# Performance work log

Hardware: AMD Instinct MI355X
Metric: run time of the kernel (lower is better)

The kernel has to match this reference:

```python
import jax, jax.numpy as jnp
import numpy as np

BATCH, N, DIM_IN, DIM_K, DIM_V, NH = 2, 4096, 256, 256, 256, 8

def setup_inputs() -> dict:
    key = jax.random.key(0)
    k1, k2, k3, k4 = jax.random.split(key, 4)
    s = 1.0 / np.sqrt(DIM_IN)
    return {
        "x": jax.random.normal(k1, (BATCH, N, DIM_IN), dtype=jnp.float32),
        "Wq": jax.random.normal(k2, (DIM_IN, DIM_K), dtype=jnp.float32) * s,
        "Wk": jax.random.normal(k3, (DIM_IN, DIM_K), dtype=jnp.float32) * s,
        "Wv": jax.random.normal(k4, (DIM_IN, DIM_V), dtype=jnp.float32) * s,
    }

def reference(x, Wq, Wk, Wv):
    b, n, _ = x.shape
    nh = NH
    dk = DIM_K // nh
    dv = DIM_V // nh
    # project and split heads: [b, nh, n, dk]
    q = jnp.einsum('bni,ik->bnk', x, Wq).reshape(b, n, nh, dk).transpose(0, 2, 1, 3)
    k = jnp.einsum('bni,ik->bnk', x, Wk).reshape(b, n, nh, dk).transpose(0, 2, 1, 3)
    v = jnp.einsum('bni,iv->bnv', x, Wv).reshape(b, n, nh, dv).transpose(0, 2, 1, 3)
    scale = 1.0 / np.sqrt(dk)
    dist = jnp.einsum('bhqd,bhkd->bhqk', q, k) * scale  # [b, nh, n, n]
    dist = jax.nn.softmax(dist, axis=-1)
    # dropout is identity in eval mode
    att = jnp.einsum('bhqk,bhkv->bhqv', dist, v)  # [b, nh, n, dv]
    return att.transpose(0, 2, 1, 3).reshape(b, n, DIM_V)
```

## Files before the change

### kernel.cpp

```cpp
#include <hip/hip_runtime.h>
#include <math.h>

#define BATCH 2
#define SEQ   4096
#define DIN   256
#define NH    8
#define DH    32
#define BH    (BATCH*NH)
#define NSPLIT 8
#define KRANGE (SEQ/NSPLIT)
#define TILES  (KRANGE/64)
#define QTILE  256

typedef short bf16x8 __attribute__((ext_vector_type(8)));
typedef float f32x4  __attribute__((ext_vector_type(4)));

#if defined(__has_builtin)
#if __has_builtin(__builtin_amdgcn_exp2f)
#define EXP2(x) __builtin_amdgcn_exp2f(x)
#else
#define EXP2_ASM 1
#endif
#else
#define EXP2_ASM 1
#endif
#ifdef EXP2_ASM
__device__ __forceinline__ float exp2_raw(float x) {
    float r;
    asm("v_exp_f32 %0, %1\n\ts_nop 1" : "=v"(r) : "v"(x));
    return r;
}
#define EXP2(x) exp2_raw(x)
#endif

#if defined(__has_builtin)
#if __has_builtin(__builtin_amdgcn_permlane32_swap) && __has_builtin(__builtin_amdgcn_permlane16_swap)
#define HAS_PERMSWAP 1
#endif
#endif

#define SC2 0.25508218f

__device__ __forceinline__ unsigned short f2bf(float f) {
    unsigned int u = __builtin_bit_cast(unsigned int, f);
    u += 0x7fffu + ((u >> 16) & 1u);
    return (unsigned short)(u >> 16);
}

__device__ __forceinline__ unsigned int pack_bf2(float f0, float f1) {
    unsigned int u0 = __builtin_bit_cast(unsigned int, f0) + 0x8000u;
    unsigned int u1 = __builtin_bit_cast(unsigned int, f1) + 0x8000u;
    return __builtin_amdgcn_perm(u1, u0, 0x07060302u);
}

__device__ __forceinline__ unsigned int pack_bf2_t(float f0, float f1) {
    return __builtin_amdgcn_perm(__builtin_bit_cast(unsigned int, f1),
                                 __builtin_bit_cast(unsigned int, f0),
                                 0x07060302u);
}

#if defined(__has_builtin)
#if __has_builtin(__builtin_amdgcn_global_load_lds)
#define HAS_ASYNC_LDS 1
#endif
#endif

__device__ __forceinline__ void stage16(const unsigned short* g,
                                        unsigned short* lds_base, int lane) {
#ifdef HAS_ASYNC_LDS
    __builtin_amdgcn_global_load_lds(
        (const __attribute__((address_space(1))) unsigned int*)g,
        (__attribute__((address_space(3))) unsigned int*)lds_base, 16, 0, 0);
#else
    *(bf16x8*)(lds_base + (size_t)lane * 8) = *(const bf16x8*)g;
#endif
}

__global__ __launch_bounds__(256) void prep_kernel(
    const float* __restrict__ Wq, const float* __restrict__ Wk, const float* __restrict__ Wv,
    unsigned short* __restrict__ Wt)
{
    __shared__ float ws[64][65];
    const int t = threadIdx.x;
    int wsel = blockIdx.x >> 4;
    int tile = blockIdx.x & 15;
    int tr = (tile >> 2) * 64;
    int tc = (tile & 3) * 64;
    const float* __restrict__ W = (wsel == 0) ? Wq : (wsel == 1) ? Wk : Wv;
    #pragma unroll
    for (int i = 0; i < 16; i++) {
        int row = i * 4 + (t >> 6), col = t & 63;
        ws[row][col] = W[(size_t)(tr + row) * DIN + tc + col];
    }
    __syncthreads();
    unsigned short* dst = Wt + (size_t)wsel * DIN * DIN;
    #pragma unroll
    for (int i = 0; i < 16; i++) {
        int orow = i * 4 + (t >> 6), ocol = t & 63;
        dst[(size_t)(tc + orow) * DIN + tr + ocol] = f2bf(ws[ocol][orow]);
    }
}

__global__ __launch_bounds__(256) void proj_kernel(
    const float* __restrict__ x, const unsigned short* __restrict__ Wt,
    unsigned short* __restrict__ qh, unsigned short* __restrict__ kh,
    unsigned short* __restrict__ vt)
{
    __shared__ __align__(16) unsigned short abuf[8][4][64][8];
    __shared__ __align__(16) unsigned short bbuf[8][4][64][8];

    const int wsel = blockIdx.y;
    const int w    = threadIdx.x >> 6;
    const int lane = threadIdx.x & 63;
    const int quad = lane >> 4;
    const int l16  = lane & 15;

    const int sl   = lane ^ (lane >> 3);
    const int sl16 = sl >> 2, squad = sl & 3;
    const int s_ = (l16 << 2) | quad;
    const int jj = (s_ & 56) | ((s_ ^ (s_ >> 3)) & 7);

    int arow0, brow0;
    const unsigned short* Wbase;
    const float* Xbase;
    unsigned short (*wdst)[4][64][8];
    unsigned short (*xdst)[4][64][8];
    if (wsel < 2) {
        int tt = blockIdx.x >> 7, nt = blockIdx.x & 127;
        arow0 = tt * 64; brow0 = nt * 64;
        Wbase = Wt + (size_t)wsel * DIN * DIN + (size_t)arow0 * DIN;
        Xbase = x + (size_t)brow0 * DIN;
        wdst = abuf; xdst = bbuf;
    } else {
        int nt = blockIdx.x >> 2, tt = blockIdx.x & 3;
        arow0 = nt * 64; brow0 = tt * 64;
        Xbase = x + (size_t)arow0 * DIN;
        Wbase = Wt + (size_t)2 * DIN * DIN + (size_t)brow0 * DIN;
        wdst = bbuf; xdst = abuf;
    }

    #pragma unroll
    for (int i = 0; i < 8; i++) {
        int id = w * 8 + i;
        int kb = id >> 2, rt = id & 3;
        stage16(Wbase + (size_t)(rt * 16 + sl16) * DIN + kb * 32 + squad * 8,
                &wdst[kb][rt][0][0], lane);
    }
    #pragma unroll
    for (int i = 0; i < 8; i++) {
        int id = w * 8 + i;
        int kb = id >> 2, rt = id & 3;
        const float4* src = (const float4*)(Xbase + (size_t)(rt * 16 + sl16) * DIN
                                            + kb * 32 + squad * 8);
        float4 a = src[0], b = src[1];
        uint4 p = { pack_bf2(a.x, a.y), pack_bf2(a.z, a.w),
                    pack_bf2(b.x, b.y), pack_bf2(b.z, b.w) };
        *(uint4*)(&xdst[kb][rt][0][0] + (size_t)lane * 8) = p;
    }
    __syncthreads();

    f32x4 acc[4];
    #pragma unroll
    for (int c = 0; c < 4; c++) acc[c] = (f32x4){0.f, 0.f, 0.f, 0.f};
    #pragma unroll
    for (int kb = 0; kb < 8; kb++) {
        bf16x8 af = *(const bf16x8*)&abuf[kb][w][jj][0];
        #pragma unroll
        for (int c = 0; c < 4; c++) {
            bf16x8 bfr = *(const bf16x8*)&bbuf[kb][c][jj][0];
            acc[c] = __builtin_amdgcn_mfma_f32_16x16x32_bf16(af, bfr, acc[c], 0, 0, 0);
        }
    }

    if (wsel < 2) {
        const float scl = (wsel == 0) ? SC2 : 1.0f;
        unsigned short* __restrict__ dst0 = (wsel == 0) ? qh : kh;
        const int t0 = arow0 + w * 16;
        const int h = t0 >> 5, d0 = (t0 & 31) + quad * 4;
        #pragma unroll
        for (int c = 0; c < 4; c++) {
            int n = brow0 + c * 16 + l16;
            int b = n >> 12, n12 = n & 4095;
            unsigned int u01 = pack_bf2(acc[c][0] * scl, acc[c][1] * scl);
            unsigned int u23 = pack_bf2(acc[c][2] * scl, acc[c][3] * scl);
            *(uint2*)&dst0[((size_t)(b * NH + h) * SEQ + n12) * DH + d0] = make_uint2(u01, u23);
        }
    } else {
        const int n0w = arow0 + w * 16;
        const int b = n0w >> 12, nbase = (n0w & 4095) + quad * 4;
        #pragma unroll
        for (int c = 0; c < 4; c++) {
            int t = brow0 + c * 16;
            int h = t >> 5, d = (t & 31) + l16;
            unsigned int u01 = pack_bf2(acc[c][0], acc[c][1]);
            unsigned int u23 = pack_bf2(acc[c][2], acc[c][3]);
            *(uint2*)&vt[((size_t)(b * NH + h) * DH + d) * SEQ + nbase] = make_uint2(u01, u23);
        }
    }
}

__global__ __launch_bounds__(256, 4) void attn_kernel(
    const unsigned short* __restrict__ qh,
    const unsigned short* __restrict__ kh,
    const unsigned short* __restrict__ vt,
    unsigned short* __restrict__ po, float* __restrict__ pl)
{
#ifndef HAS_PERMSWAP
    __shared__ __align__(16) unsigned short pbuf[4][2][16][64];
#endif
    __shared__ __align__(16) unsigned short kbuf[2][4][64][8];
    __shared__ __align__(16) unsigned short vbuf[2][4][64][8];

    const int tid  = threadIdx.x;
    const int wave = tid >> 6;
    const int lane = tid & 63;
    const int quad = lane >> 4;
    const int l16  = lane & 15;

    const int bh = blockIdx.x & 15;
    const int qb = (blockIdx.x >> 4) & 15;
    const int ks = blockIdx.x >> 8;
    const int q0 = qb * QTILE + wave * 64;
    const int kbase = ks * KRANGE;

    const unsigned short* __restrict__ Qp = qh + (size_t)bh * SEQ * DH;
    const unsigned short* __restrict__ Kp = kh + (size_t)bh * SEQ * DH;
    const unsigned short* __restrict__ Vp = vt + (size_t)bh * DH * SEQ;

    const int sl    = lane ^ (lane >> 3);
    const int sl16  = sl >> 2, squad = sl & 3;
    const unsigned short* ksrc = Kp + (size_t)(kbase + wave * 16 + sl16) * DH + squad * 8;
    const int vdh = wave >> 1, vkh = wave & 1;
    const unsigned short* vsrc = Vp + (size_t)(vdh * 16 + sl16) * SEQ + kbase + vkh * 32 + squad * 8;

    const int s_ = (l16 << 2) | quad;
    const int jj = (s_ & 56) | ((s_ ^ (s_ >> 3)) & 7);

    bf16x8 qf[4];
    #pragma unroll
    for (int i = 0; i < 4; i++)
        qf[i] = *(const bf16x8*)(Qp + (size_t)(q0 + i * 16 + l16) * DH + quad * 8);

    const bf16x8 ones = {0x3F80, 0x3F80, 0x3F80, 0x3F80,
                         0x3F80, 0x3F80, 0x3F80, 0x3F80};

    f32x4 o[4][2];
    f32x4 lones[4];
    #pragma unroll
    for (int i = 0; i < 4; i++) {
        o[i][0] = (f32x4){0.f, 0.f, 0.f, 0.f};
        o[i][1] = (f32x4){0.f, 0.f, 0.f, 0.f};
        lones[i] = (f32x4){0.f, 0.f, 0.f, 0.f};
    }
    const f32x4 z = {0.f, 0.f, 0.f, 0.f};

    stage16(ksrc, &kbuf[0][wave][0][0], lane);
    stage16(vsrc, &vbuf[0][wave][0][0], lane);
    ksrc += 64 * DH;
    vsrc += 64;

    for (int t = 0; t < TILES; t++) {
        const int buf = t & 1;

        __syncthreads();

        if (t + 1 < TILES) {
            stage16(ksrc, &kbuf[buf ^ 1][wave][0][0], lane);
            stage16(vsrc, &vbuf[buf ^ 1][wave][0][0], lane);
            ksrc += 64 * DH;
            vsrc += 64;
        }

        bf16x8 kf[4], vf[4];
        #pragma unroll
        for (int c = 0; c < 4; c++) kf[c] = *(const bf16x8*)&kbuf[buf][c][jj][0];
        #pragma unroll
        for (int f = 0; f < 4; f++) vf[f] = *(const bf16x8*)&vbuf[buf][f][jj][0];

        #pragma unroll
        for (int qt = 0; qt < 4; qt++) {
#ifdef HAS_PERMSWAP
            unsigned int w0[2], w1[2], w2[2], w3[2];
            #pragma unroll
            for (int c = 0; c < 4; c++) {
                f32x4 s = __builtin_amdgcn_mfma_f32_16x16x32_bf16(kf[c], qf[qt], z, 0, 0, 0);
                unsigned int lo = pack_bf2_t(EXP2(s[0]), EXP2(s[1]));
                unsigned int hi = pack_bf2_t(EXP2(s[2]), EXP2(s[3]));
                if      (c == 0) { w0[0] = lo; w0[1] = hi; }
                else if (c == 1) { w1[0] = lo; w1[1] = hi; }
                else if (c == 2) { w2[0] = lo; w2[1] = hi; }
                else             { w3[0] = lo; w3[1] = hi; }
            }
            uint4 f0, f1;
            {
                typedef unsigned int u32x2 __attribute__((ext_vector_type(2)));
                u32x2 a, b;
                a = __builtin_amdgcn_permlane32_swap(w0[0], w1[0], false, false);
                b = __builtin_amdgcn_permlane16_swap(a.x, a.y, false, false);
                f0.x = b.x; f0.z = b.y;
                a = __builtin_amdgcn_permlane32_swap(w0[1], w1[1], false, false);
                b = __builtin_amdgcn_permlane16_swap(a.x, a.y, false, false);
                f0.y = b.x; f0.w = b.y;
                a = __builtin_amdgcn_permlane32_swap(w2[0], w3[0], false, false);
                b = __builtin_amdgcn_permlane16_swap(a.x, a.y, false, false);
                f1.x = b.x; f1.z = b.y;
                a = __builtin_amdgcn_permlane32_swap(w2[1], w3[1], false, false);
                b = __builtin_amdgcn_permlane16_swap(a.x, a.y, false, false);
                f1.y = b.x; f1.w = b.y;
            }
            bf16x8 pf0 = __builtin_bit_cast(bf16x8, f0);
            bf16x8 pf1 = __builtin_bit_cast(bf16x8, f1);
#else
            const int sw = l16 & 7;
            const int pr = qt & 1;
            #pragma unroll
            for (int c = 0; c < 4; c++) {
                f32x4 s = __builtin_amdgcn_mfma_f32_16x16x32_bf16(kf[c], qf[qt], z, 0, 0, 0);
                float e0 = EXP2(s[0]);
                float e1 = EXP2(s[1]);
                float e2 = EXP2(s[2]);
                float e3 = EXP2(s[3]);
                int chs = ((c * 2 + (quad >> 1)) ^ sw) * 8 + (quad & 1) * 4;
                *(uint2*)&pbuf[wave][pr][l16][chs] =
                    make_uint2(pack_bf2_t(e0, e1), pack_bf2_t(e2, e3));
            }
            bf16x8 pf0 = *(const bf16x8*)&pbuf[wave][pr][l16][((0 + quad) ^ sw) * 8];
            bf16x8 pf1 = *(const bf16x8*)&pbuf[wave][pr][l16][((4 + quad) ^ sw) * 8];
#endif
            __builtin_amdgcn_s_setprio(1);
            o[qt][0] = __builtin_amdgcn_mfma_f32_16x16x32_bf16(pf0, vf[0], o[qt][0], 0, 0, 0);
            o[qt][0] = __builtin_amdgcn_mfma_f32_16x16x32_bf16(pf1, vf[1], o[qt][0], 0, 0, 0);
            o[qt][1] = __builtin_amdgcn_mfma_f32_16x16x32_bf16(pf0, vf[2], o[qt][1], 0, 0, 0);
            o[qt][1] = __builtin_amdgcn_mfma_f32_16x16x32_bf16(pf1, vf[3], o[qt][1], 0, 0, 0);
            lones[qt] = __builtin_amdgcn_mfma_f32_16x16x32_bf16(pf0, ones, lones[qt], 0, 0, 0);
            lones[qt] = __builtin_amdgcn_mfma_f32_16x16x32_bf16(pf1, ones, lones[qt], 0, 0, 0);
            __builtin_amdgcn_s_setprio(0);
        }
    }

    const size_t obase = (size_t)(ks * BH + bh) * SEQ;
    #pragma unroll
    for (int qt = 0; qt < 4; qt++) {
        if (l16 == 0) {
            #pragma unroll
            for (int r = 0; r < 4; r++)
                pl[obase + q0 + qt * 16 + quad * 4 + r] = lones[qt][r];
        }
        #pragma unroll
        for (int r = 0; r < 4; r++) {
            int n = q0 + qt * 16 + quad * 4 + r;
            unsigned short* dst = po + (obase + n) * DH;
            dst[l16]      = f2bf(o[qt][0][r]);
            dst[16 + l16] = f2bf(o[qt][1][r]);
        }
    }
}

__global__ __launch_bounds__(256) void merge_kernel(
    const unsigned short* __restrict__ po, const float* __restrict__ pl,
    float* __restrict__ out)
{
    int t    = blockIdx.x * 256 + threadIdx.x;
    int d8   = t & 7;
    int pair = t >> 3;
    int bh   = pair >> 12;
    int n    = pair & 4095;
    float s0 = 0.f, s1 = 0.f, s2 = 0.f, s3 = 0.f, ls = 0.f;
    #pragma unroll
    for (int sp = 0; sp < NSPLIT; sp++) {
        size_t base = (size_t)(sp * BH + bh) * SEQ + n;
        uint2 v = ((const uint2*)(po + base * DH))[d8];
        s0 += __builtin_bit_cast(float, v.x << 16);
        s1 += __builtin_bit_cast(float, v.x & 0xFFFF0000u);
        s2 += __builtin_bit_cast(float, v.y << 16);
        s3 += __builtin_bit_cast(float, v.y & 0xFFFF0000u);
        ls += pl[base];
    }
    float inv = 1.f / ls;
    int b = bh >> 3, h = bh & 7;
    float4 o = {s0 * inv, s1 * inv, s2 * inv, s3 * inv};
    ((float4*)(out + ((size_t)b * SEQ + n) * (NH * DH) + h * DH))[d8] = o;
}

extern "C" void kernel_launch(void* const* d_in, const int* in_sizes, int n_in,
                              void* d_out, int out_size, void* d_ws, size_t ws_size,
                              hipStream_t stream)
{
    const float* x  = (const float*)d_in[0];
    const float* Wq = (const float*)d_in[1];
    const float* Wk = (const float*)d_in[2];
    const float* Wv = (const float*)d_in[3];
    float* out = (float*)d_out;

    unsigned short* qh = (unsigned short*)d_ws;
    unsigned short* kh = qh + (size_t)BH * SEQ * DH;
    unsigned short* vt = kh + (size_t)BH * SEQ * DH;
    unsigned short* Wt = vt + (size_t)BH * SEQ * DH;
    unsigned short* po = Wt + 3 * DIN * DIN;
    float* pl = (float*)(po + (size_t)NSPLIT * BH * SEQ * DH);

    prep_kernel<<<dim3(48), 256, 0, stream>>>(Wq, Wk, Wv, Wt);
    proj_kernel<<<dim3(512, 3), 256, 0, stream>>>(x, Wt, qh, kh, vt);
    attn_kernel<<<dim3(BH * (SEQ / QTILE) * NSPLIT), 256, 0, stream>>>(qh, kh, vt, po, pl);
    merge_kernel<<<dim3(2048), 256, 0, stream>>>(po, pl, out);
}
```

Before: 137.2 us.

## Halve key splits and stage two key tiles per barrier interval

Cuts the key-range split count from 8 to 4, so each block covers a key range twice as long. K/V are now staged in pairs of 64-row tiles per double-buffered interval, which halves the number of __syncthreads per tile processed. The grid shrinks by half, so there is less parallelism on the GPU, fewer partial outputs to combine, and more shared memory per block. Whether the combine kernel and grid indexing (blockIdx >> 8 for ks) stay consistent depends on the code not shown.

Result: faster. 133.7 us (-2.6%).

```diff
diff --git a/kernel.cpp b/kernel.cpp
--- a/kernel.cpp
+++ b/kernel.cpp
@@ -7,9 +7,9 @@
 #define NH    8
 #define DH    32
 #define BH    (BATCH*NH)
-#define NSPLIT 8
+#define NSPLIT 4
 #define KRANGE (SEQ/NSPLIT)
-#define TILES  (KRANGE/64)
+#define NIV   (KRANGE/128)
 #define QTILE  256
 
 typedef short bf16x8 __attribute__((ext_vector_type(8)));
@@ -208,8 +208,8 @@
 #ifndef HAS_PERMSWAP
     __shared__ __align__(16) unsigned short pbuf[4][2][16][64];
 #endif
-    __shared__ __align__(16) unsigned short kbuf[2][4][64][8];
-    __shared__ __align__(16) unsigned short vbuf[2][4][64][8];
+    __shared__ __align__(16) unsigned short kbuf[2][2][4][64][8];
+    __shared__ __align__(16) unsigned short vbuf[2][2][4][64][8];
 
     const int tid  = threadIdx.x;
     const int wave = tid >> 6;
@@ -254,87 +254,94 @@
     }
     const f32x4 z = {0.f, 0.f, 0.f, 0.f};
 
-    stage16(ksrc, &kbuf[0][wave][0][0], lane);
-    stage16(vsrc, &vbuf[0][wave][0][0], lane);
-    ksrc += 64 * DH;
-    vsrc += 64;
-
-    for (int t = 0; t < TILES; t++) {
-        const int buf = t & 1;
+    stage16(ksrc,           &kbuf[0][0][wave][0][0], lane);
+    stage16(ksrc + 64 * DH, &kbuf[0][1][wave][0][0], lane);
+    stage16(vsrc,           &vbuf[0][0][wave][0][0], lane);
+    stage16(vsrc + 64,      &vbuf[0][1][wave][0][0], lane);
+    ksrc += 128 * DH;
+    vsrc += 128;
+
+    for (int iv = 0; iv < NIV; iv++) {
+        const int buf = iv & 1;
 
         __syncthreads();
 
-        if (t + 1 < TILES) {
-            stage16(ksrc, &kbuf[buf ^ 1][wave][0][0], lane);
-            stage16(vsrc, &vbuf[buf ^ 1][wave][0][0], lane);
-            ksrc += 64 * DH;
-            vsrc += 64;
-        }
-
-        bf16x8 kf[4], vf[4];
+        if (iv + 1 < NIV) {
+            stage16(ksrc,           &kbuf[buf ^ 1][0][wave][0][0], lane);
+            stage16(ksrc + 64 * DH, &kbuf[buf ^ 1][1][wave][0][0], lane);
+            stage16(vsrc,           &vbuf[buf ^ 1][0][wave][0][0], lane);
+            stage16(vsrc + 64,      &vbuf[buf ^ 1][1][wave][0][0], lane);
+            ksrc += 128 * DH;
+            vsrc += 128;
+        }
+
         #pragma unroll
-        for (int c = 0; c < 4; c++) kf[c] = *(const bf16x8*)&kbuf[buf][c][jj][0];
-        #pragma unroll
-        for (int f = 0; f < 4; f++) vf[f] = *(const bf16x8*)&vbuf[buf][f][jj][0];
-
-        #pragma unroll
-        for (int qt = 0; qt < 4; qt++) {
+        for (int h = 0; h < 2; h++) {
+            bf16x8 kf[4], vf[4];
+            #pragma unroll
+            for (int c = 0; c < 4; c++) kf[c] = *(const bf16x8*)&kbuf[buf][h][c][jj][0];
+            #pragma unroll
+            for (int f = 0; f < 4; f++) vf[f] = *(const bf16x8*)&vbuf[buf][h][f][jj][0];
+
+            #pragma unroll
+            for (int qt = 0; qt < 4; qt++) {
 #ifdef HAS_PERMSWAP
-            unsigned int w0[2], w1[2], w2[2], w3[2];
-            #pragma unroll
-            for (int c = 0; c < 4; c++) {
-                f32x4 s = __builtin_amdgcn_mfma_f32_16x16x32_bf16(kf[c], qf[qt], z, 0, 0, 0);
-                unsigned int lo = pack_bf2_t(EXP2(s[0]), EXP2(s[1]));
-                unsigned int hi = pack_bf2_t(EXP2(s[2]), EXP2(s[3]));
-                if      (c == 0) { w0[0] = lo; w0[1] = hi; }
-                else if (c == 1) { w1[0] = lo; w1[1] = hi; }
-                else if (c == 2) { w2[0] = lo; w2[1] = hi; }
-                else             { w3[0] = lo; w3[1] = hi; }
+                unsigned int w0[2], w1[2], w2[2], w3[2];
+                #pragma unroll
+                for (int c = 0; c < 4; c++) {
+                    f32x4 s = __builtin_amdgcn_mfma_f32_16x16x32_bf16(kf[c], qf[qt], z, 0, 0, 0);
+                    unsigned int lo = pack_bf2_t(EXP2(s[0]), EXP2(s[1]));
+                    unsigned int hi = pack_bf2_t(EXP2(s[2]), EXP2(s[3]));
+                    if      (c == 0) { w0[0] = lo; w0[1] = hi; }
+                    else if (c == 1) { w1[0] = lo; w1[1] = hi; }
+                    else if (c == 2) { w2[0] = lo; w2[1] = hi; }
+                    else             { w3[0] = lo; w3[1] = hi; }
+                }
+                uint4 f0, f1;
+                {
+                    typedef unsigned int u32x2 __attribute__((ext_vector_type(2)));
+                    u32x2 a, b;
+                    a = __builtin_amdgcn_permlane32_swap(w0[0], w1[0], false, false);
+                    b = __builtin_amdgcn_permlane16_swap(a.x, a.y, false, false);
+                    f0.x = b.x; f0.z = b.y;
+                    a = __builtin_amdgcn_permlane32_swap(w0[1], w1[1], false, false);
+                    b = __builtin_amdgcn_permlane16_swap(a.x, a.y, false, false);
+                    f0.y = b.x; f0.w = b.y;
+                    a = __builtin_amdgcn_permlane32_swap(w2[0], w3[0], false, false);
+                    b = __builtin_amdgcn_permlane16_swap(a.x, a.y, false, false);
+                    f1.x = b.x; f1.z = b.y;
+                    a = __builtin_amdgcn_permlane32_swap(w2[1], w3[1], false, false);
+                    b = __builtin_amdgcn_permlane16_swap(a.x, a.y, false, false);
+                    f1.y = b.x; f1.w = b.y;
+                }
+                bf16x8 pf0 = __builtin_bit_cast(bf16x8, f0);
+                bf16x8 pf1 = __builtin_bit_cast(bf16x8, f1);
+#else
+                const int sw = l16 & 7;
+                const int pr = qt & 1;
+                #pragma unroll
+                for (int c = 0; c < 4; c++) {
+                    f32x4 s = __builtin_amdgcn_mfma_f32_16x16x32_bf16(kf[c], qf[qt], z, 0, 0, 0);
+                    float e0 = EXP2(s[0]);
+                    float e1 = EXP2(s[1]);
+                    float e2 = EXP2(s[2]);
+                    float e3 = EXP2(s[3]);
+                    int chs = ((c * 2 + (quad >> 1)) ^ sw) * 8 + (quad & 1) * 4;
+                    *(uint2*)&pbuf[wave][pr][l16][chs] =
+                        make_uint2(pack_bf2_t(e0, e1), pack_bf2_t(e2, e3));
+                }
+                bf16x8 pf0 = *(const bf16x8*)&pbuf[wave][pr][l16][((0 + quad) ^ sw) * 8];
+                bf16x8 pf1 = *(const bf16x8*)&pbuf[wave][pr][l16][((4 + quad) ^ sw) * 8];
+#endif
+                __builtin_amdgcn_s_setprio(1);
+                o[qt][0] = __builtin_amdgcn_mfma_f32_16x16x32_bf16(pf0, vf[0], o[qt][0], 0, 0, 0);
+                o[qt][0] = __builtin_amdgcn_mfma_f32_16x16x32_bf16(pf1, vf[1], o[qt][0], 0, 0, 0);
+                o[qt][1] = __builtin_amdgcn_mfma_f32_16x16x32_bf16(pf0, vf[2], o[qt][1], 0, 0, 0);
+                o[qt][1] = __builtin_amdgcn_mfma_f32_16x16x32_bf16(pf1, vf[3], o[qt][1], 0, 0, 0);
+                lones[qt] = __builtin_amdgcn_mfma_f32_16x16x32_bf16(pf0, ones, lones[qt], 0, 0, 0);
+                lones[qt] = __builtin_amdgcn_mfma_f32_16x16x32_bf16(pf1, ones, lones[qt], 0, 0, 0);
+                __builtin_amdgcn_s_setprio(0);
             }
-            uint4 f0, f1;
-            {
-                typedef unsigned int u32x2 __attribute__((ext_vector_type(2)));
-                u32x2 a, b;
-                a = __builtin_amdgcn_permlane32_swap(w0[0], w1[0], false, false);
-                b = __builtin_amdgcn_permlane16_swap(a.x, a.y, false, false);
-                f0.x = b.x; f0.z = b.y;
-                a = __builtin_amdgcn_permlane32_swap(w0[1], w1[1], false, false);
-                b = __builtin_amdgcn_permlane16_swap(a.x, a.y, false, false);
-                f0.y = b.x; f0.w = b.y;
-                a = __builtin_amdgcn_permlane32_swap(w2[0], w3[0], false, false);
-                b = __builtin_amdgcn_permlane16_swap(a.x, a.y, false, false);
-                f1.x = b.x; f1.z = b.y;
-                a = __builtin_amdgcn_permlane32_swap(w2[1], w3[1], false, false);
-                b = __builtin_amdgcn_permlane16_swap(a.x, a.y, false, false);
-                f1.y = b.x; f1.w = b.y;
-            }
-            bf16x8 pf0 = __builtin_bit_cast(bf16x8, f0);
-            bf16x8 pf1 = __builtin_bit_cast(bf16x8, f1);
-#else
-            const int sw = l16 & 7;
-            const int pr = qt & 1;
-            #pragma unroll
-            for (int c = 0; c < 4; c++) {
-                f32x4 s = __builtin_amdgcn_mfma_f32_16x16x32_bf16(kf[c], qf[qt], z, 0, 0, 0);
-                float e0 = EXP2(s[0]);
-                float e1 = EXP2(s[1]);
-                float e2 = EXP2(s[2]);
-                float e3 = EXP2(s[3]);
-                int chs = ((c * 2 + (quad >> 1)) ^ sw) * 8 + (quad & 1) * 4;
-                *(uint2*)&pbuf[wave][pr][l16][chs] =
-                    make_uint2(pack_bf2_t(e0, e1), pack_bf2_t(e2, e3));
-            }
-            bf16x8 pf0 = *(const bf16x8*)&pbuf[wave][pr][l16][((0 + quad) ^ sw) * 8];
-            bf16x8 pf1 = *(const bf16x8*)&pbuf[wave][pr][l16][((4 + quad) ^ sw) * 8];
-#endif
-            __builtin_amdgcn_s_setprio(1);
-            o[qt][0] = __builtin_amdgcn_mfma_f32_16x16x32_bf16(pf0, vf[0], o[qt][0], 0, 0, 0);
-            o[qt][0] = __builtin_amdgcn_mfma_f32_16x16x32_bf16(pf1, vf[1], o[qt][0], 0, 0, 0);
-            o[qt][1] = __builtin_amdgcn_mfma_f32_16x16x32_bf16(pf0, vf[2], o[qt][1], 0, 0, 0);
-            o[qt][1] = __builtin_amdgcn_mfma_f32_16x16x32_bf16(pf1, vf[3], o[qt][1], 0, 0, 0);
-            lones[qt] = __builtin_amdgcn_mfma_f32_16x16x32_bf16(pf0, ones, lones[qt], 0, 0, 0);
-            lones[qt] = __builtin_amdgcn_mfma_f32_16x16x32_bf16(pf1, ones, lones[qt], 0, 0, 0);
-            __builtin_amdgcn_s_setprio(0);
         }
     }
 
```
